# Kernel optimization log

Measured on AMD Instinct MI355X. Metric: run time of the kernel, lower is better.

## Reference

```python
import jax, jax.numpy as jnp
import numpy as np

N = 50000      # nodes
E = 1600000    # edges (before self loops)
IN = 128       # in_channels
HID = 64       # hidden_channels
OUT = 16       # out_channels
NEG_SLOPE = 0.2


def gat_conv(x, edge_index, W, a_src, a_dst, bias, heads, ch):
    """PyG GATConv: linear -> per-edge attention (LeakyReLU) -> segment softmax
    over destination nodes -> scatter-add aggregation. add_self_loops=True."""
    n = x.shape[0]
    loop = jnp.arange(n, dtype=edge_index.dtype)
    src = jnp.concatenate([edge_index[0], loop])  # [Etot]
    dst = jnp.concatenate([edge_index[1], loop])
    h = (x @ W).reshape(n, heads, ch)             # [N,H,C]
    asrc = jnp.sum(h * a_src, axis=-1)            # [N,H]
    adst = jnp.sum(h * a_dst, axis=-1)            # [N,H]
    e = jax.nn.leaky_relu(asrc[src] + adst[dst], NEG_SLOPE)      # [Etot,H]
    emax = jax.ops.segment_max(e, dst, num_segments=n)           # [N,H]
    emax = jnp.where(jnp.isfinite(emax), emax, 0.0)
    p = jnp.exp(e - emax[dst])
    denom = jax.ops.segment_sum(p, dst, num_segments=n)          # [N,H]
    alpha = p / (denom[dst] + 1e-16)                             # [Etot,H]
    out = jax.ops.segment_sum(h[src] * alpha[:, :, None], dst, num_segments=n)
    return out.reshape(n, heads * ch) + bias      # concat (heads=1 is a no-op)


def setup_inputs() -> dict:
    key = jax.random.key(0)
    ks = jax.random.split(key, 12)
    s = 0.05
    return {
        "x": jax.random.normal(ks[0], (N, IN), dtype=jnp.float32),
        "edge_index": jax.random.randint(ks[1], (2, E), 0, N, dtype=jnp.int64),
        # conv1: heads=2
        "W1": jax.random.normal(ks[2], (IN, 2 * HID), dtype=jnp.float32) * s,
        "a_src1": jax.random.normal(ks[3], (2, HID), dtype=jnp.float32) * s,
        "a_dst1": jax.random.normal(ks[4], (2, HID), dtype=jnp.float32) * s,
        "b1": jnp.zeros((2 * HID,), dtype=jnp.float32),
        # conv2: heads=1, in = 2*HID
        "W2": jax.random.normal(ks[5], (2 * HID, HID), dtype=jnp.float32) * s,
        "a_src2": jax.random.normal(ks[6], (1, HID), dtype=jnp.float32) * s,
        "a_dst2": jax.random.normal(ks[7], (1, HID), dtype=jnp.float32) * s,
        "b2": jnp.zeros((HID,), dtype=jnp.float32),
        # final linear
        "Wl": jax.random.normal(ks[8], (HID, OUT), dtype=jnp.float32) * s,
        "bl": jnp.zeros((OUT,), dtype=jnp.float32),
    }


def reference(x, edge_index, W1, a_src1, a_dst1, b1, W2, a_src2, a_dst2, b2, Wl, bl):
    h = jax.nn.relu(gat_conv(x, edge_index, W1, a_src1, a_dst1, b1, heads=2, ch=HID))
    # dropout p=0.3: identity at inference (deterministic reference)
    h = jax.nn.relu(gat_conv(h, edge_index, W2, a_src2, a_dst2, b2, heads=1, ch=HID))
    return h @ Wl + bl
```

## Files before the change

### kernel.cpp

```cpp
#include <hip/hip_runtime.h>
#include <hip/hip_fp16.h>

#define NEG 0.2f
#define RW 512
#define RSH 9
#define RCAP 18432


template <int K, int M, int H, bool PART>
__global__ __launch_bounds__(256) void k_gemm(const float* __restrict__ X,
                                              const float* __restrict__ W,
                                              const float* __restrict__ a_src,
                                              const float* __restrict__ a_dst,
                                              __half* __restrict__ Yh,
                                              float* __restrict__ asrc,
                                              float* __restrict__ adst, int n,
                                              const int* __restrict__ esrc,
                                              const int* __restrict__ edst, int E, int NRg,
                                              int* rcur, unsigned int* part) {
    constexpr int KH = 32;
    __shared__ float Ws[KH * M];
    __shared__ float Xs[32][K + 4];
    int tid = threadIdx.x;
    int row0 = blockIdx.x * 32;

    if (PART && blockIdx.x * 2048 < E) {
        __shared__ int ph[128];
        __shared__ int pb[128];
        int i0 = (blockIdx.x * 256 + tid) * 8;
        int ds[8], ss[8];
        if (i0 + 7 < E) {
            int4 a = *reinterpret_cast<const int4*>(&edst[i0]);
            int4 b = *reinterpret_cast<const int4*>(&edst[i0 + 4]);
            ds[0] = a.x; ds[1] = a.y; ds[2] = a.z; ds[3] = a.w;
            ds[4] = b.x; ds[5] = b.y; ds[6] = b.z; ds[7] = b.w;
            int4 c = *reinterpret_cast<const int4*>(&esrc[i0]);
            int4 d = *reinterpret_cast<const int4*>(&esrc[i0 + 4]);
            ss[0] = c.x; ss[1] = c.y; ss[2] = c.z; ss[3] = c.w;
            ss[4] = d.x; ss[5] = d.y; ss[6] = d.z; ss[7] = d.w;
        } else {
#pragma unroll
            for (int j = 0; j < 8; j++) {
                ds[j] = (i0 + j < E) ? edst[i0 + j] : 0;
                ss[j] = (i0 + j < E) ? esrc[i0 + j] : 0;
            }
        }
        if (tid < NRg) ph[tid] = 0;
        __syncthreads();
#pragma unroll
        for (int j = 0; j < 8; j++)
            if (i0 + j < E) atomicAdd(&ph[ds[j] >> RSH], 1);
        __syncthreads();
        if (tid < NRg) {
            int c = ph[tid];
            pb[tid] = c ? atomicAdd(&rcur[tid], c) : 0;
            ph[tid] = 0;
        }
        __syncthreads();
#pragma unroll
        for (int j = 0; j < 8; j++) {
            if (i0 + j < E) {
                int r = ds[j] >> RSH;
                int rk = atomicAdd(&ph[r], 1) + pb[r];
                if (rk < RCAP)
                    part[(size_t)r * RCAP + rk] =
                        ((unsigned int)(ds[j] & (RW - 1)) << 16) | (unsigned int)(ss[j] & 0xFFFF);
            }
        }
    }

    for (int idx = tid; idx < 32 * (K / 4); idx += 256) {
        int r = idx / (K / 4), c4 = idx % (K / 4);
        int gr = row0 + r;
        float4 v = make_float4(0.f, 0.f, 0.f, 0.f);
        if (gr < n) v = *reinterpret_cast<const float4*>(&X[(size_t)gr * K + c4 * 4]);
        *reinterpret_cast<float4*>(&Xs[r][c4 * 4]) = v;
    }

    constexpr int NJ = M / 32;
    float4 acc[NJ];
#pragma unroll
    for (int j = 0; j < NJ; j++) acc[j] = make_float4(0.f, 0.f, 0.f, 0.f);
    int r = tid >> 3, cg = tid & 7;

    for (int kh = 0; kh < K; kh += KH) {
        __syncthreads();
        for (int idx = tid; idx < (KH * M) / 4; idx += 256) {
            *reinterpret_cast<float4*>(&Ws[idx * 4]) =
                *reinterpret_cast<const float4*>(&W[(size_t)kh * M + idx * 4]);
        }
        __syncthreads();
        for (int k = 0; k < KH; k++) {
            float xv = Xs[r][kh + k];
#pragma unroll
            for (int j = 0; j < NJ; j++) {
                float4 wv = *reinterpret_cast<const float4*>(&Ws[k * M + cg * 4 + j * 32]);
                acc[j].x += xv * wv.x;
                acc[j].y += xv * wv.y;
                acc[j].z += xv * wv.z;
                acc[j].w += xv * wv.w;
            }
        }
    }

    int gr = row0 + r;
    if (gr < n) {
#pragma unroll
        for (int j = 0; j < NJ; j++) {
            union {
                __half2 h2[2];
                uint2 u;
            } cv;
            cv.h2[0] = __floats2half2_rn(acc[j].x, acc[j].y);
            cv.h2[1] = __floats2half2_rn(acc[j].z, acc[j].w);
            *reinterpret_cast<uint2*>(&Yh[(size_t)gr * M + cg * 4 + j * 32]) = cv.u;
        }
    }

    float ps0 = 0.f, pd0 = 0.f, ps1 = 0.f, pd1 = 0.f;
#pragma unroll
    for (int j = 0; j < NJ; j++) {
        int colb = cg * 4 + j * 32;
        float4 av = *reinterpret_cast<const float4*>(&a_src[colb]);
        float4 dv = *reinterpret_cast<const float4*>(&a_dst[colb]);
        float s = acc[j].x * av.x + acc[j].y * av.y + acc[j].z * av.z + acc[j].w * av.w;
        float d = acc[j].x * dv.x + acc[j].y * dv.y + acc[j].z * dv.z + acc[j].w * dv.w;
        if (H == 2 && j >= NJ / 2) {
            ps1 += s;
            pd1 += d;
        } else {
            ps0 += s;
            pd0 += d;
        }
    }
#pragma unroll
    for (int m = 1; m < 8; m <<= 1) {
        ps0 += __shfl_xor(ps0, m, 64);
        pd0 += __shfl_xor(pd0, m, 64);
        if (H == 2) {
            ps1 += __shfl_xor(ps1, m, 64);
            pd1 += __shfl_xor(pd1, m, 64);
        }
    }
    if (gr < n && cg == 0) {
        if (H == 2) {
            *reinterpret_cast<float2*>(&asrc[gr * 2]) = make_float2(ps0, ps1);
            *reinterpret_cast<float2*>(&adst[gr * 2]) = make_float2(pd0, pd1);
        } else {
            asrc[gr] = ps0;
            adst[gr] = pd0;
        }
    }
}


__global__ __launch_bounds__(512) void k_build(const unsigned int* __restrict__ part,
                                               const int* __restrict__ rcur, int n,
                                               unsigned short* __restrict__ csr,
                                               int* __restrict__ rowptr) {
    __shared__ int hist[RW];
    __shared__ int wsum[8];
    __shared__ int rbase_s;
    int r = blockIdx.x;
    int tid = threadIdx.x, lane = tid & 63, wid = tid >> 6;
    int cnt = min(rcur[r], RCAP);
    if (tid == 0) {
        int b = 0;
        for (int j = 0; j < r; j++) b += min(rcur[j], RCAP);
        rbase_s = b;
    }
    hist[tid] = 0;
    __syncthreads();
    int rbase = rbase_s;
    const unsigned int* pr = part + (size_t)r * RCAP;

    for (int i = tid; i < cnt; i += 512) atomicAdd(&hist[pr[i] >> 16], 1);
    __syncthreads();

    int v = hist[tid];
    int incl = v;
#pragma unroll
    for (int m = 1; m < 64; m <<= 1) {
        int t = __shfl_up(incl, m, 64);
        if (lane >= m) incl += t;
    }
    if (lane == 63) wsum[wid] = incl;
    __syncthreads();
    if (wid == 0) {
        int s = (lane < 8) ? wsum[lane] : 0;
#pragma unroll
        for (int m = 1; m < 8; m <<= 1) {
            int t = __shfl_up(s, m, 64);
            if (lane >= m) s += t;
        }
        if (lane < 8) wsum[lane] = s;
    }
    __syncthreads();
    int excl = (incl - v) + (wid > 0 ? wsum[wid - 1] : 0);
    __syncthreads();
    hist[tid] = excl;
    int g = r * RW + tid;
    if (g < n) rowptr[g] = rbase + excl;
    if (r == gridDim.x - 1 && tid == 0) rowptr[n] = rbase + cnt;
    __syncthreads();

    for (int i = tid; i < cnt; i += 512) {
        unsigned int e = pr[i];
        int rk = atomicAdd(&hist[e >> 16], 1);
        csr[rbase + rk] = (unsigned short)(e & 0xFFFF);
    }
}


__global__ __launch_bounds__(256) void k_gat2(const __half* __restrict__ hh,
                                              const float* __restrict__ asrc,
                                              const float* __restrict__ adst,
                                              const int* __restrict__ rowptr,
                                              const unsigned short* __restrict__ csr_src,
                                              const float* __restrict__ bias,
                                              float* __restrict__ out, int n) {
    int node = blockIdx.x * 4 + (threadIdx.x >> 6);
    int lane = threadIdx.x & 63;
    if (node >= n) return;

    int beg = rowptr[node], end = rowptr[node + 1];
    float2 adn = *reinterpret_cast<const float2*>(&adst[node * 2]);
    float2 asn = *reinterpret_cast<const float2*>(&asrc[node * 2]);
    float e0 = asn.x + adn.x;
    e0 = e0 > 0.f ? e0 : NEG * e0;
    float e1 = asn.y + adn.y;
    e1 = e1 > 0.f ? e1 : NEG * e1;
    float pself0 = __expf(e0), pself1 = __expf(e1);

    int g = lane >> 4;
    int lc = lane & 15;
    bool head1 = lc >= 8;

    float4 sraw = *reinterpret_cast<const float4*>(&hh[(size_t)node * 128 + lc * 8]);

    float2 acc[4];
#pragma unroll
    for (int k = 0; k < 4; k++) acc[k] = make_float2(0.f, 0.f);
    float psum0 = 0.f, psum1 = 0.f;

    for (int base = beg; base < end; base += 64) {
        int i = base + lane;
        int cnt = min(64, end - base);
        float p0 = 0.f, p1 = 0.f;
        int s = 0;
        if (i < end) {
            s = (int)csr_src[i];
            float2 a2 = *reinterpret_cast<const float2*>(&asrc[s * 2]);
            float f0 = a2.x + adn.x;
            f0 = f0 > 0.f ? f0 : NEG * f0;
            float f1 = a2.y + adn.y;
            f1 = f1 > 0.f ? f1 : NEG * f1;
            p0 = __expf(f0);
            p1 = __expf(f1);
            psum0 += p0;
            psum1 += p1;
        }
        int nt = (cnt + 3) >> 2;
#pragma unroll 8
        for (int t = 0; t < nt; t++) {
            int ej = t * 4 + g;
            int sj = __shfl(s, ej, 64);
            float pj0 = __shfl(p0, ej, 64);
            float pj1 = __shfl(p1, ej, 64);
            float pj = head1 ? pj1 : pj0;
            if (ej < cnt) {
                float4 raw = *reinterpret_cast<const float4*>(&hh[(size_t)sj * 128 + lc * 8]);
                const __half2* hp = reinterpret_cast<const __half2*>(&raw);
#pragma unroll
                for (int k = 0; k < 4; k++) {
                    float2 f = __half22float2(hp[k]);
                    acc[k].x += pj * f.x;
                    acc[k].y += pj * f.y;
                }
            }
        }
    }

#pragma unroll
    for (int m = 1; m < 64; m <<= 1) {
        psum0 += __shfl_xor(psum0, m, 64);
        psum1 += __shfl_xor(psum1, m, 64);
    }
    float inv0 = 1.f / (psum0 + pself0 + 1e-16f);
    float inv1 = 1.f / (psum1 + pself1 + 1e-16f);

#pragma unroll
    for (int m = 16; m < 64; m <<= 1) {
#pragma unroll
        for (int k = 0; k < 4; k++) {
            acc[k].x += __shfl_xor(acc[k].x, m, 64);
            acc[k].y += __shfl_xor(acc[k].y, m, 64);
        }
    }

    float inv = head1 ? inv1 : inv0;
    float pself = head1 ? pself1 : pself0;
    const __half2* sp = reinterpret_cast<const __half2*>(&sraw);
    float4 b0 = *reinterpret_cast<const float4*>(&bias[lc * 8]);
    float4 b1 = *reinterpret_cast<const float4*>(&bias[lc * 8 + 4]);
    float o[8];
#pragma unroll
    for (int k = 0; k < 4; k++) {
        float2 f = __half22float2(sp[k]);
        o[2 * k] = (acc[k].x + pself * f.x) * inv;
        o[2 * k + 1] = (acc[k].y + pself * f.y) * inv;
    }
    o[0] = fmaxf(o[0] + b0.x, 0.f);
    o[1] = fmaxf(o[1] + b0.y, 0.f);
    o[2] = fmaxf(o[2] + b0.z, 0.f);
    o[3] = fmaxf(o[3] + b0.w, 0.f);
    o[4] = fmaxf(o[4] + b1.x, 0.f);
    o[5] = fmaxf(o[5] + b1.y, 0.f);
    o[6] = fmaxf(o[6] + b1.z, 0.f);
    o[7] = fmaxf(o[7] + b1.w, 0.f);

    if (lane < 16) {
        float* op = &out[(size_t)node * 128 + lc * 8];
        *reinterpret_cast<float4*>(op) = make_float4(o[0], o[1], o[2], o[3]);
        *reinterpret_cast<float4*>(op + 4) = make_float4(o[4], o[5], o[6], o[7]);
    }
}


__global__ __launch_bounds__(256) void k_gat1(const __half* __restrict__ hh,
                                              const float* __restrict__ asrc,
                                              const float* __restrict__ adst,
                                              const int* __restrict__ rowptr,
                                              const unsigned short* __restrict__ csr_src,
                                              const float* __restrict__ bias,
                                              const float* __restrict__ Wl,
                                              const float* __restrict__ bl,
                                              float* __restrict__ out, int n) {
    __shared__ float Wls[64 * 16];
    __shared__ float bls[16];
    __shared__ float hbuf[4][64];
    int tid = threadIdx.x;
    for (int i = tid; i < 64 * 16; i += 256) Wls[i] = Wl[i];
    if (tid < 16) bls[tid] = bl[tid];
    __syncthreads();

    int w = tid >> 6, lane = tid & 63;
    int node = blockIdx.x * 4 + w;
    if (node >= n) return;

    int beg = rowptr[node], end = rowptr[node + 1];
    float adn = adst[node];
    float e0 = asrc[node] + adn;
    e0 = e0 > 0.f ? e0 : NEG * e0;
    float pself = __expf(e0);

    int g = lane >> 3;
    int lc = lane & 7;

    float4 sraw = *reinterpret_cast<const float4*>(&hh[(size_t)node * 64 + lc * 8]);

    float2 acc[4];
#pragma unroll
    for (int k = 0; k < 4; k++) acc[k] = make_float2(0.f, 0.f);
    float psum = 0.f;

    for (int base = beg; base < end; base += 64) {
        int i = base + lane;
        int cnt = min(64, end - base);
        float p = 0.f;
        int s = 0;
        if (i < end) {
            s = (int)csr_src[i];
            float e = asrc[s] + adn;
            e = e > 0.f ? e : NEG * e;
            p = __expf(e);
            psum += p;
        }
        int nt = (cnt + 7) >> 3;
#pragma unroll 8
        for (int t = 0; t < nt; t++) {
            int ej = t * 8 + g;
            int sj = __shfl(s, ej, 64);
            float pj = __shfl(p, ej, 64);
            if (ej < cnt) {
                float4 raw = *reinterpret_cast<const float4*>(&hh[(size_t)sj * 64 + lc * 8]);
                const __half2* hp = reinterpret_cast<const __half2*>(&raw);
#pragma unroll
                for (int k = 0; k < 4; k++) {
                    float2 f = __half22float2(hp[k]);
                    acc[k].x += pj * f.x;
                    acc[k].y += pj * f.y;
                }
            }
        }
    }

#pragma unroll
    for (int m = 1; m < 64; m <<= 1) psum += __shfl_xor(psum, m, 64);
    float inv = 1.f / (psum + pself + 1e-16f);

#pragma unroll
    for (int m = 8; m < 64; m <<= 1) {
#pragma unroll
        for (int k = 0; k < 4; k++) {
            acc[k].x += __shfl_xor(acc[k].x, m, 64);
            acc[k].y += __shfl_xor(acc[k].y, m, 64);
        }
    }

    const __half2* sp = reinterpret_cast<const __half2*>(&sraw);
    float4 b0 = *reinterpret_cast<const float4*>(&bias[lc * 8]);
    float4 b1 = *reinterpret_cast<const float4*>(&bias[lc * 8 + 4]);
    float o[8];
#pragma unroll
    for (int k = 0; k < 4; k++) {
        float2 f = __half22float2(sp[k]);
        o[2 * k] = (acc[k].x + pself * f.x) * inv;
        o[2 * k + 1] = (acc[k].y + pself * f.y) * inv;
    }
    o[0] = fmaxf(o[0] + b0.x, 0.f);
    o[1] = fmaxf(o[1] + b0.y, 0.f);
    o[2] = fmaxf(o[2] + b0.z, 0.f);
    o[3] = fmaxf(o[3] + b0.w, 0.f);
    o[4] = fmaxf(o[4] + b1.x, 0.f);
    o[5] = fmaxf(o[5] + b1.y, 0.f);
    o[6] = fmaxf(o[6] + b1.z, 0.f);
    o[7] = fmaxf(o[7] + b1.w, 0.f);

    if (lane < 8) {
        float* hp = &hbuf[w][lc * 8];
        *reinterpret_cast<float4*>(hp) = make_float4(o[0], o[1], o[2], o[3]);
        *reinterpret_cast<float4*>(hp + 4) = make_float4(o[4], o[5], o[6], o[7]);
    }
    __builtin_amdgcn_wave_barrier();

    int col = lane & 15, q = lane >> 4;
    float a = 0.f;
#pragma unroll
    for (int k = 0; k < 16; k++) {
        int kk = q * 16 + k;
        a += hbuf[w][kk] * Wls[kk * 16 + col];
    }
    a += __shfl_xor(a, 16, 64);
    a += __shfl_xor(a, 32, 64);
    if (lane < 16) out[(size_t)node * 16 + col] = a + bls[col];
}


extern "C" void kernel_launch(void* const* d_in, const int* in_sizes, int n_in,
                              void* d_out, int out_size, void* d_ws, size_t ws_size,
                              hipStream_t stream) {
    const float* x      = (const float*)d_in[0];
    const int*   ei     = (const int*)d_in[1];
    const float* W1     = (const float*)d_in[2];
    const float* a_src1 = (const float*)d_in[3];
    const float* a_dst1 = (const float*)d_in[4];
    const float* b1     = (const float*)d_in[5];
    const float* W2     = (const float*)d_in[6];
    const float* a_src2 = (const float*)d_in[7];
    const float* a_dst2 = (const float*)d_in[8];
    const float* b2     = (const float*)d_in[9];
    const float* Wl     = (const float*)d_in[10];
    const float* bl     = (const float*)d_in[11];
    float* out = (float*)d_out;

    int n = in_sizes[0] / 128;
    int E = in_sizes[1] / 2;
    const int* src = ei;
    const int* dst = ei + E;
    int NRg = (n + RW - 1) >> RSH;

    char* w = (char*)d_ws;
    size_t off = 0;
    auto alloc = [&](size_t bytes) {
        void* p = w + off;
        off = (off + bytes + 255) & ~(size_t)255;
        return p;
    };
    int*            rcur   = (int*)alloc(128 * 4);
    unsigned int*   part   = (unsigned int*)alloc((size_t)NRg * RCAP * 4);
    int*            rowptr = (int*)alloc((size_t)(n + 1) * 4);
    unsigned short* csr    = (unsigned short*)alloc((size_t)E * 2);
    __half*         h1h    = (__half*)alloc((size_t)n * 128 * 2);
    float*          as1    = (float*)alloc((size_t)n * 2 * 4);
    float*          ad1    = (float*)alloc((size_t)n * 2 * 4);
    float*          hm     = (float*)alloc((size_t)n * 128 * 4);
    __half*         h2h    = (__half*)alloc((size_t)n * 64 * 2);
    float*          as2    = (float*)alloc((size_t)n * 4);
    float*          ad2    = (float*)alloc((size_t)n * 4);

    hipMemsetAsync(rcur, 0, 128 * 4, stream);

    int gblocks = (n + 31) / 32;
    int bblocks = (E + 2047) / 2048;
    int grid1 = gblocks > bblocks ? gblocks : bblocks;

    k_gemm<128, 128, 2, true><<<grid1, 256, 0, stream>>>(x, W1, a_src1, a_dst1, h1h, as1, ad1, n,
                                                         src, dst, E, NRg, rcur, part);
    k_build<<<NRg, 512, 0, stream>>>(part, rcur, n, csr, rowptr);
    k_gat2<<<(n + 3) / 4, 256, 0, stream>>>(h1h, as1, ad1, rowptr, csr, b1, hm, n);

    k_gemm<128, 64, 1, false><<<gblocks, 256, 0, stream>>>(hm, W2, a_src2, a_dst2, h2h, as2, ad2, n,
                                                           nullptr, nullptr, 0, 0, nullptr, nullptr);
    k_gat1<<<(n + 3) / 4, 256, 0, stream>>>(h2h, as2, ad2, rowptr, csr, b2, Wl, bl, out, n);
}
```

Before: 225.4 us.

## Use fp16 MFMA for GAT linear layers and store intermediate features in half

Replaces the scalar FP32 GEMM with MFMA 16x16x32 f16 instructions, using a new prep kernel that transposes and converts W1/W2 to half. The edge-partition work is split into separate interleaved blocks instead of sharing blocks with the GEMM. The layer-1 aggregation output is now written in fp16, which halves the traffic for the second GEMM's input. Attention logits are computed from the fp16-rounded tile, which adds precision loss, and there is one extra kernel launch.

```diff
diff --git a/kernel.cpp b/kernel.cpp
--- a/kernel.cpp
+++ b/kernel.cpp
@@ -6,28 +6,65 @@
 #define RSH 9
 #define RCAP 18432
 
-
-template <int K, int M, int H, bool PART>
-__global__ __launch_bounds__(256) void k_gemm(const float* __restrict__ X,
-                                              const float* __restrict__ W,
+typedef _Float16 f16x8 __attribute__((ext_vector_type(8)));
+typedef float f32x4 __attribute__((ext_vector_type(4)));
+
+__device__ __forceinline__ unsigned int pack2(float lo, float hi) {
+    union { __half2 h; unsigned int u; } cv;
+    cv.h = __floats2half2_rn(lo, hi);
+    return cv.u;
+}
+
+
+__global__ __launch_bounds__(256) void k_prep(const float* __restrict__ W1,
+                                              const float* __restrict__ W2,
+                                              __half* __restrict__ Wt1, __half* __restrict__ Wt2) {
+    __shared__ float tile[64][65];
+    int b = blockIdx.x;
+    const float* W;
+    __half* Wt;
+    int Mw, kt, mt;
+    if (b < 4) { W = W1; Wt = Wt1; Mw = 128; kt = b >> 1; mt = b & 1; }
+    else       { W = W2; Wt = Wt2; Mw = 64;  kt = b - 4;  mt = 0; }
+    int tid = threadIdx.x;
+    for (int i = tid; i < 4096; i += 256) {
+        int kr = i >> 6, mc = i & 63;
+        tile[kr][mc] = W[(size_t)(kt * 64 + kr) * Mw + mt * 64 + mc];
+    }
+    __syncthreads();
+    for (int i = tid; i < 512; i += 256) {
+        int m = i >> 3, c8 = i & 7;
+        __half tmp[8];
+#pragma unroll
+        for (int j = 0; j < 8; j++) tmp[j] = (__half)tile[c8 * 8 + j][m];
+        *reinterpret_cast<uint4*>(&Wt[(size_t)(mt * 64 + m) * 128 + kt * 64 + c8 * 8]) =
+            *reinterpret_cast<uint4*>(tmp);
+    }
+}
+
+
+template <int K, int M, int H, bool PART, bool XHALF>
+__global__ __launch_bounds__(256) void k_gemm(const void* __restrict__ Xv,
+                                              const __half* __restrict__ Wt,
                                               const float* __restrict__ a_src,
                                               const float* __restrict__ a_dst,
                                               __half* __restrict__ Yh,
                                               float* __restrict__ asrc,
                                               float* __restrict__ adst, int n,
                                               const int* __restrict__ esrc,
-                                              const int* __restrict__ edst, int E, int NRg,
+                                              const int* __restrict__ edst, int E,
+                                              int NRg, int gemmCount, int partCount,
                                               int* rcur, unsigned int* part) {
-    constexpr int KH = 32;
-    __shared__ float Ws[KH * M];
-    __shared__ float Xs[32][K + 4];
+    constexpr int NT = M / 32;
+    __shared__ __half htile[32][M + 4];
     int tid = threadIdx.x;
-    int row0 = blockIdx.x * 32;
-
-    if (PART && blockIdx.x * 2048 < E) {
+    int bix = PART ? (blockIdx.x >> 1) : blockIdx.x;
+
+    if (PART && (blockIdx.x & 1)) {
+        if (bix >= partCount) return;
         __shared__ int ph[128];
         __shared__ int pb[128];
-        int i0 = (blockIdx.x * 256 + tid) * 8;
+        int i0 = (bix * 256 + tid) * 8;
         int ds[8], ss[8];
         if (i0 + 7 < E) {
             int4 a = *reinterpret_cast<const int4*>(&edst[i0]);
@@ -67,88 +104,106 @@
                         ((unsigned int)(ds[j] & (RW - 1)) << 16) | (unsigned int)(ss[j] & 0xFFFF);
             }
         }
-    }
-
-    for (int idx = tid; idx < 32 * (K / 4); idx += 256) {
-        int r = idx / (K / 4), c4 = idx % (K / 4);
+        return;
+    }
+    if (PART && bix >= gemmCount) return;
+    int row0 = bix * 32;
+
+    int w4 = tid >> 6, lane = tid & 63;
+    int rt = w4 & 1;
+    int ct0 = (w4 >> 1) * NT;
+    int lrow = lane & 15, lk = lane >> 4;
+    int grow = row0 + rt * 16 + lrow;
+
+    f32x4 acc[NT];
+#pragma unroll
+    for (int i = 0; i < NT; i++) acc[i] = (f32x4){0.f, 0.f, 0.f, 0.f};
+
+#pragma unroll 1
+    for (int s = 0; s < K / 32; s++) {
+        int kbase = s * 32 + lk * 8;
+        f16x8 af;
+        if (XHALF) {
+            const __half* Xh = (const __half*)Xv;
+            union { uint4 u; f16x8 v; } cv;
+            cv.u = make_uint4(0u, 0u, 0u, 0u);
+            if (grow < n) cv.u = *reinterpret_cast<const uint4*>(&Xh[(size_t)grow * K + kbase]);
+            af = cv.v;
+        } else {
+            const float* X = (const float*)Xv;
+            if (grow < n) {
+                float4 a = *reinterpret_cast<const float4*>(&X[(size_t)grow * K + kbase]);
+                float4 b = *reinterpret_cast<const float4*>(&X[(size_t)grow * K + kbase + 4]);
+                af[0] = (_Float16)a.x; af[1] = (_Float16)a.y;
+                af[2] = (_Float16)a.z; af[3] = (_Float16)a.w;
+                af[4] = (_Float16)b.x; af[5] = (_Float16)b.y;
+                af[6] = (_Float16)b.z; af[7] = (_Float16)b.w;
+            } else {
+#pragma unroll
+                for (int j = 0; j < 8; j++) af[j] = (_Float16)0.f;
+            }
+        }
+#pragma unroll
+        for (int i = 0; i < NT; i++) {
+            int col = (ct0 + i) * 16 + lrow;
+            union { uint4 u; f16x8 v; } bc;
+            bc.u = *reinterpret_cast<const uint4*>(&Wt[(size_t)col * K + kbase]);
+            acc[i] = __builtin_amdgcn_mfma_f32_16x16x32_f16(af, bc.v, acc[i], 0, 0, 0);
+        }
+    }
+
+#pragma unroll
+    for (int i = 0; i < NT; i++) {
+        int col = (ct0 + i) * 16 + lrow;
+#pragma unroll
+        for (int j = 0; j < 4; j++) {
+            int rl = rt * 16 + lk * 4 + j;
+            htile[rl][col] = (__half)acc[i][j];
+        }
+    }
+    __syncthreads();
+
+    for (int idx = tid; idx < 32 * (M / 8); idx += 256) {
+        int r = idx / (M / 8), c8 = idx % (M / 8);
         int gr = row0 + r;
-        float4 v = make_float4(0.f, 0.f, 0.f, 0.f);
-        if (gr < n) v = *reinterpret_cast<const float4*>(&X[(size_t)gr * K + c4 * 4]);
-        *reinterpret_cast<float4*>(&Xs[r][c4 * 4]) = v;
-    }
-
-    constexpr int NJ = M / 32;
-    float4 acc[NJ];
-#pragma unroll
-    for (int j = 0; j < NJ; j++) acc[j] = make_float4(0.f, 0.f, 0.f, 0.f);
-    int r = tid >> 3, cg = tid & 7;
-
-    for (int kh = 0; kh < K; kh += KH) {
-        __syncthreads();
-        for (int idx = tid; idx < (KH * M) / 4; idx += 256) {
-            *reinterpret_cast<float4*>(&Ws[idx * 4]) =
-                *reinterpret_cast<const float4*>(&W[(size_t)kh * M + idx * 4]);
-        }
-        __syncthreads();
-        for (int k = 0; k < KH; k++) {
-            float xv = Xs[r][kh + k];
-#pragma unroll
-            for (int j = 0; j < NJ; j++) {
-                float4 wv = *reinterpret_cast<const float4*>(&Ws[k * M + cg * 4 + j * 32]);
-                acc[j].x += xv * wv.x;
-                acc[j].y += xv * wv.y;
-                acc[j].z += xv * wv.z;
-                acc[j].w += xv * wv.w;
-            }
-        }
-    }
-
-    int gr = row0 + r;
-    if (gr < n) {
-#pragma unroll
-        for (int j = 0; j < NJ; j++) {
-            union {
-                __half2 h2[2];
-                uint2 u;
-            } cv;
-            cv.h2[0] = __floats2half2_rn(acc[j].x, acc[j].y);
-            cv.h2[1] = __floats2half2_rn(acc[j].z, acc[j].w);
-            *reinterpret_cast<uint2*>(&Yh[(size_t)gr * M + cg * 4 + j * 32]) = cv.u;
-        }
-    }
-
-    float ps0 = 0.f, pd0 = 0.f, ps1 = 0.f, pd1 = 0.f;
-#pragma unroll
-    for (int j = 0; j < NJ; j++) {
-        int colb = cg * 4 + j * 32;
-        float4 av = *reinterpret_cast<const float4*>(&a_src[colb]);
-        float4 dv = *reinterpret_cast<const float4*>(&a_dst[colb]);
-        float s = acc[j].x * av.x + acc[j].y * av.y + acc[j].z * av.z + acc[j].w * av.w;
-        float d = acc[j].x * dv.x + acc[j].y * dv.y + acc[j].z * dv.z + acc[j].w * dv.w;
-        if (H == 2 && j >= NJ / 2) {
-            ps1 += s;
-            pd1 += d;
-        } else {
-            ps0 += s;
-            pd0 += d;
-        }
-    }
-#pragma unroll
-    for (int m = 1; m < 8; m <<= 1) {
-        ps0 += __shfl_xor(ps0, m, 64);
-        pd0 += __shfl_xor(pd0, m, 64);
-        if (H == 2) {
-            ps1 += __shfl_xor(ps1, m, 64);
-            pd1 += __shfl_xor(pd1, m, 64);
-        }
-    }
-    if (gr < n && cg == 0) {
-        if (H == 2) {
-            *reinterpret_cast<float2*>(&asrc[gr * 2]) = make_float2(ps0, ps1);
-            *reinterpret_cast<float2*>(&adst[gr * 2]) = make_float2(pd0, pd1);
-        } else {
-            asrc[gr] = ps0;
-            adst[gr] = pd0;
+        if (gr < n)
+            *reinterpret_cast<uint4*>(&Yh[(size_t)gr * M + c8 * 8]) =
+                *reinterpret_cast<const uint4*>(&htile[r][c8 * 8]);
+    }
+
+    if (H == 2) {
+        int row = tid >> 3, part = tid & 7;
+        int gr = row0 + row;
+        float s = 0.f, d = 0.f;
+#pragma unroll
+        for (int j = 0; j < 16; j++) {
+            float hv = (float)htile[row][part * 16 + j];
+            s += hv * a_src[part * 16 + j];
+            d += hv * a_dst[part * 16 + j];
+        }
+        s += __shfl_xor(s, 1, 64); d += __shfl_xor(d, 1, 64);
+        s += __shfl_xor(s, 2, 64); d += __shfl_xor(d, 2, 64);
+        if (gr < n && (part & 3) == 0) {
+            asrc[gr * 2 + (part >> 2)] = s;
+            adst[gr * 2 + (part >> 2)] = d;
+        }
+    } else {
+        if (tid < 128) {
+            int row = tid >> 2, part = tid & 3;
+            int gr = row0 + row;
+            float s = 0.f, d = 0.f;
+#pragma unroll
+            for (int j = 0; j < 16; j++) {
+                float hv = (float)htile[row][part * 16 + j];
+                s += hv * a_src[part * 16 + j];
+                d += hv * a_dst[part * 16 + j];
+            }
+            s += __shfl_xor(s, 1, 64); d += __shfl_xor(d, 1, 64);
+            s += __shfl_xor(s, 2, 64); d += __shfl_xor(d, 2, 64);
+            if (gr < n && part == 0) {
+                asrc[gr] = s;
+                adst[gr] = d;
+            }
         }
     }
 }
@@ -218,7 +273,7 @@
                                               const int* __restrict__ rowptr,
                                               const unsigned short* __restrict__ csr_src,
                                               const float* __restrict__ bias,
-                                              float* __restrict__ out, int n) {
+                                              __half* __restrict__ outh, int n) {
     int node = blockIdx.x * 4 + (threadIdx.x >> 6);
     int lane = threadIdx.x & 63;
     if (node >= n) return;
@@ -320,9 +375,12 @@
     o[7] = fmaxf(o[7] + b1.w, 0.f);
 
     if (lane < 16) {
-        float* op = &out[(size_t)node * 128 + lc * 8];
-        *reinterpret_cast<float4*>(op) = make_float4(o[0], o[1], o[2], o[3]);
-        *reinterpret_cast<float4*>(op + 4) = make_float4(o[4], o[5], o[6], o[7]);
+        uint4 cv;
+        cv.x = pack2(o[0], o[1]);
+        cv.y = pack2(o[2], o[3]);
+        cv.z = pack2(o[4], o[5]);
+        cv.w = pack2(o[6], o[7]);
+        *reinterpret_cast<uint4*>(&outh[(size_t)node * 128 + lc * 8]) = cv;
     }
 }
 
@@ -481,10 +539,12 @@
     unsigned int*   part   = (unsigned int*)alloc((size_t)NRg * RCAP * 4);
     int*            rowptr = (int*)alloc((size_t)(n + 1) * 4);
     unsigned short* csr    = (unsigned short*)alloc((size_t)E * 2);
+    __half*         wt1    = (__half*)alloc(128 * 128 * 2);
+    __half*         wt2    = (__half*)alloc(64 * 128 * 2);
     __half*         h1h    = (__half*)alloc((size_t)n * 128 * 2);
     float*          as1    = (float*)alloc((size_t)n * 2 * 4);
     float*          ad1    = (float*)alloc((size_t)n * 2 * 4);
-    float*          hm     = (float*)alloc((size_t)n * 128 * 4);
+    __half*         hmh    = (__half*)alloc((size_t)n * 128 * 2);
     __half*         h2h    = (__half*)alloc((size_t)n * 64 * 2);
     float*          as2    = (float*)alloc((size_t)n * 4);
     float*          ad2    = (float*)alloc((size_t)n * 4);
@@ -493,14 +553,16 @@
 
     int gblocks = (n + 31) / 32;
     int bblocks = (E + 2047) / 2048;
-    int grid1 = gblocks > bblocks ? gblocks : bblocks;
-
-    k_gemm<128, 128, 2, true><<<grid1, 256, 0, stream>>>(x, W1, a_src1, a_dst1, h1h, as1, ad1, n,
-                                                         src, dst, E, NRg, rcur, part);
+    int half = gblocks > bblocks ? gblocks : bblocks;
+
+    k_prep<<<6, 256, 0, stream>>>(W1, W2, wt1, wt2);
+
+    k_gemm<128, 128, 2, true, false><<<2 * half, 256, 0, stream>>>(
+        x, wt1, a_src1, a_dst1, h1h, as1, ad1, n, src, dst, E, NRg, gblocks, bblocks, rcur, part);
     k_build<<<NRg, 512, 0, stream>>>(part, rcur, n, csr, rowptr);
-    k_gat2<<<(n + 3) / 4, 256, 0, stream>>>(h1h, as1, ad1, rowptr, csr, b1, hm, n);
-
-    k_gemm<128, 64, 1, false><<<gblocks, 256, 0, stream>>>(hm, W2, a_src2, a_dst2, h2h, as2, ad2, n,
-                                                           nullptr, nullptr, 0, 0, nullptr, nullptr);
+    k_gat2<<<(n + 3) / 4, 256, 0, stream>>>(h1h, as1, ad1, rowptr, csr, b1, hmh, n);
+
+    k_gemm<128, 64, 1, false, true><<<gblocks, 256, 0, stream>>>(
+        hmh, wt2, a_src2, a_dst2, h2h, as2, ad2, n, nullptr, nullptr, 0, 0, 0, 0, nullptr, nullptr);
     k_gat1<<<(n + 3) / 4, 256, 0, stream>>>(h2h, as2, ad2, rowptr, csr, b2, Wl, bl, out, n);
 }
```

Measured after the change: 193.0 us. 1.17x faster.
